# Performance work log

Hardware: AMD Instinct MI355X
Metric: run time of the kernel (lower is better)

## Reference

```python
import jax, jax.numpy as jnp
import numpy as np

B, L, H = 256, 2048, 64

def _min_gru(x, Wz, bz, Wh, bh):
    # x: [B, L, Din] -> h: [B, L, H] via parallel scan of h_t = (1-z_t)*h_{t-1} + z_t*h~_t, h_0 = 0
    z = jax.nn.sigmoid(jnp.einsum('bli,ih->blh', x, Wz) + bz)
    h_tilde = jnp.einsum('bli,ih->blh', x, Wh) + bh
    a = 1.0 - z
    b = z * h_tilde
    def combine(c1, c2):
        a1, b1 = c1
        a2, b2 = c2
        return a1 * a2, b1 * a2 + b2
    _, h = jax.lax.associative_scan(combine, (a, b), axis=1)
    return h

def _stacked(x, Wz0, bz0, Wh0, bh0, Wz1, bz1, Wh1, bh1, Wo, bo):
    h = _min_gru(x, Wz0, bz0, Wh0, bh0)
    h = _min_gru(h, Wz1, bz1, Wh1, bh1)
    return jnp.einsum('blh,ho->blo', h, Wo) + bo  # [B, L, 1]

def setup_inputs():
    key = jax.random.key(0)
    ks = jax.random.split(key, 32)
    inputs = jax.random.bernoulli(ks[0], 0.5, (B, L)).astype(jnp.float32)
    p_array = jax.random.permutation(ks[1], L).astype(jnp.int32)
    def lin(k, fin, fout):
        return (jax.random.normal(k, (fin, fout), jnp.float32) / np.float32(np.sqrt(fin)))
    d = {'inputs': inputs, 'p_array': p_array}
    i = 2
    for r in (1, 2):
        for nm, fin, fout in (('z0', 1, H), ('h0', 1, H), ('z1', H, H), ('h1', H, H), ('o', H, 1)):
            d['w%d%s' % (r, nm)] = lin(ks[i], fin, fout); i += 1
            d['b%d%s' % (r, nm)] = jnp.zeros((fout,), jnp.float32)
    return d

def reference(inputs, p_array, w1z0, b1z0, w1h0, b1h0, w1z1, b1z1, w1h1, b1h1, w1o, b1o,
              w2z0, b2z0, w2h0, b2h0, w2z1, b2z1, w2h1, b2h1, w2o, b2o):
    x = inputs[..., None]                      # [B, L, 1]
    x_sys = _stacked(x, w1z0, b1z0, w1h0, b1h0, w1z1, b1z1, w1h1, b1h1, w1o, b1o)
    x_int = x[:, p_array, :]                   # interleave along sequence dim
    x_p1 = _stacked(x_int, w2z0, b2z0, w2h0, b2h0, w2z1, b2z1, w2h1, b2h1, w2o, b2o)
    x_tx = jnp.concatenate([x_sys, x_p1], axis=2)  # [B, L, 2]
    mean = jnp.mean(x_tx)
    std = jnp.std(x_tx, ddof=1)                # torch.std is unbiased by default
    return (x_tx - mean) / std                 # squeeze(dim=2) is a no-op on size-2 dim
```

## Files before the change

kernel.cpp:

```cpp
#include <hip/hip_runtime.h>

#define BB 256
#define LL 2048
#define HH 64
#define TT 64
#define SS 68
#define NCH (LL / TT)
#define NTOT (BB * LL * 2)

typedef __attribute__((ext_vector_type(8))) short bf16x8;
typedef __attribute__((ext_vector_type(4))) float f32x4;

__device__ __forceinline__ float rcp_(float x) { return __builtin_amdgcn_rcpf(x); }

__device__ __forceinline__ short f2bf_rne(float f) {
    union { float f; unsigned u; } v; v.f = f;
    unsigned r = v.u + 0x7fff + ((v.u >> 16) & 1);
    return (short)(r >> 16);
}

__device__ __forceinline__ unsigned perm_hi16(float f_hi, float f_lo) {
    union { float f; unsigned u; } a, b;
    a.f = f_hi; b.f = f_lo;
    return __builtin_amdgcn_perm(a.u, b.u, 0x07060302u);
}

template<int D>
__device__ __forceinline__ float rshr(float x) {
    union { float f; int i; } u, r;
    u.f = x;
    r.i = __builtin_amdgcn_update_dpp(0, u.i, 0x110 | D, 0xF, 0xF, true);
    return r.f;
}

__device__ __forceinline__ void p1_scan(const unsigned* __restrict__ bw, int c,
                                        float a0v, float b0v, float a1v, float b1v,
                                        int seg, int col0, int lane7,
                                        float& carry, float* sh)
{
    const unsigned bits = (bw[c * 2 + (seg >> 2)] >> ((seg & 3) << 3)) & 0xffu;
    float A = 1.0f, Bv = 0.0f;
    #pragma unroll
    for (int i = 0; i < 8; ++i) {
        const bool on = (bits >> i) & 1u;
        const float a = on ? a1v : a0v;
        const float b = on ? b1v : b0v;
        A  = A * a;
        Bv = fmaf(Bv, a, b);
    }
    {
        const float Au = rshr<1>(A), Bu = rshr<1>(Bv);
        if (seg >= 1) { const float Ac = A; A = Au * Ac; Bv = fmaf(Bu, Ac, Bv); }
    }
    {
        const float Au = rshr<2>(A), Bu = rshr<2>(Bv);
        if (seg >= 2) { const float Ac = A; A = Au * Ac; Bv = fmaf(Bu, Ac, Bv); }
    }
    {
        const float Au = rshr<4>(A), Bu = rshr<4>(Bv);
        if (seg >= 4) { const float Ac = A; A = Au * Ac; Bv = fmaf(Bu, Ac, Bv); }
    }
    float Ae = rshr<1>(A), Be = rshr<1>(Bv);
    if (seg == 0) { Ae = 1.0f; Be = 0.0f; }
    float cc = fmaf(Ae, carry, Be);
    #pragma unroll
    for (int i = 0; i < 8; ++i) {
        const bool on = (bits >> i) & 1u;
        const float a = on ? a1v : a0v;
        const float b = on ? b1v : b0v;
        cc = fmaf(a, cc, b);
        sh[(seg * 8 + i) * SS + col0] = cc;
    }
    carry = __shfl(cc, lane7);
}

__global__ void __launch_bounds__(512)
__attribute__((amdgpu_waves_per_eu(4, 4)))
gru_fused(const float* __restrict__ x, const int* __restrict__ p,
               const float* __restrict__ w1z0, const float* __restrict__ b1z0,
               const float* __restrict__ w1h0, const float* __restrict__ b1h0,
               const float* __restrict__ w1z1, const float* __restrict__ b1z1,
               const float* __restrict__ w1h1, const float* __restrict__ b1h1,
               const float* __restrict__ w1o,  const float* __restrict__ b1o,
               const float* __restrict__ w2z0, const float* __restrict__ b2z0,
               const float* __restrict__ w2h0, const float* __restrict__ b2h0,
               const float* __restrict__ w2z1, const float* __restrict__ b2z1,
               const float* __restrict__ w2h1, const float* __restrict__ b2h1,
               const float* __restrict__ w2o,  const float* __restrict__ b2o,
               float* __restrict__ out, float* __restrict__ ws)
{
    const int  b  = blockIdx.x;
    const bool pm = (blockIdx.y != 0);

    const float* wz0 = pm ? w2z0 : w1z0;
    const float* bz0 = pm ? b2z0 : b1z0;
    const float* wh0 = pm ? w2h0 : w1h0;
    const float* bh0 = pm ? b2h0 : b1h0;
    const float* wz1 = pm ? w2z1 : w1z1;
    const float* bz1 = pm ? b2z1 : b1z1;
    const float* wh1 = pm ? w2h1 : w1h1;
    const float* bh1 = pm ? b2h1 : b1h1;
    const float* wo  = pm ? w2o  : w1o;
    const float* bov = pm ? b2o  : b1o;

    const int tid   = threadIdx.x;
    const int lane  = tid & 63;
    const int tg    = tid >> 6;
    const int tw    = tg & 3;
    const int hw    = tg >> 2;
    const int q     = lane >> 4;
    const int n     = lane & 15;
    const int seg   = lane & 7;
    const int hidx  = (tg << 3) | (lane >> 3);
    const int lane7 = lane | 7;

    __shared__ __align__(16) float s_h[2 * TT * SS];
    __shared__ unsigned long long s_xb[LL / 64];
    __shared__ float2 s_w[2][2][4][32];
    __shared__ float s_o[2][4][16];
    __shared__ float s_red[16];

    const float* xrow = x + (size_t)b * LL;

    #pragma unroll
    for (int g = 0; g < 4; ++g) {
        const int idx = g * 512 + tid;
        const int src = pm ? p[idx] : idx;
        const unsigned long long m = __ballot(xrow[src] != 0.0f);
        if (lane == 0) s_xb[g * 8 + tg] = m;
    }
    const unsigned* bw = (const unsigned*)s_xb;

    const float z0v = rcp_(1.0f + __expf(-bz0[hidx]));
    const float z1v = rcp_(1.0f + __expf(-(wz0[hidx] + bz0[hidx])));
    const float a0v = 1.0f - z0v, b0v = z0v * bh0[hidx];
    const float a1v = 1.0f - z1v, b1v = z1v * (wh0[hidx] + bh0[hidx]);

    float rbz1[2], rbh1[2], rwo4[2];
    #pragma unroll
    for (int ht = 0; ht < 2; ++ht) {
        const int h = hw * 32 + ht * 16 + n;
        rbz1[ht] = bz1[h];
        rbh1[ht] = bh1[h];
        rwo4[ht] = wo[h];
    }
    const float bo = bov[0];

    bf16x8 wfz[2][2], wfh[2][2];
    for (int ks = 0; ks < 2; ++ks) {
        for (int ht = 0; ht < 2; ++ht) {
            #pragma unroll
            for (int j = 0; j < 8; ++j) {
                const int kk = ks * 32 + q * 8 + j;
                const int h  = hw * 32 + ht * 16 + n;
                wfz[ks][ht][j] = f2bf_rne(wz1[kk * HH + h]);
                wfh[ks][ht][j] = f2bf_rne(wh1[kk * HH + h]);
            }
        }
    }

    float carry0 = 0.0f;
    float carry1[2] = {0.0f, 0.0f};
    f32x4 ga[2], gb[2];
    float Aqe[2], Bqe[2];
    float pvo[4] = {0, 0, 0, 0};
    float lsum = 0.0f, lsum2 = 0.0f;
    float* outp = out + (pm ? 1 : 0);
    const int t0 = tw * 16;
    const int col0 = hidx ^ (seg << 2);
    const int sswz = (tw * 2 + (n >> 3)) << 2;

    auto g2_step = [&](int cm) {
        if (cm > 0 && hw == 0 && n == 15) {
            #pragma unroll
            for (int r = 0; r < 4; ++r) {
                const float v = pvo[r] + s_o[(cm - 1) & 1][tw][q * 4 + r] + bo;
                outp[((size_t)b * LL + (cm - 1) * TT + t0 + q * 4 + r) * 2] = v;
                lsum += v;
                lsum2 = fmaf(v, v, lsum2);
            }
        }
        const int buf = cm & 1;
        float Acm[2] = {1, 1}, Bcm[2] = {0, 0};
        float Ap[2], Bp[2];
        #pragma unroll
        for (int w = 0; w < 4; ++w) {
            #pragma unroll
            for (int ht = 0; ht < 2; ++ht) {
                if (w == tw) { Ap[ht] = Acm[ht]; Bp[ht] = Bcm[ht]; }
                const float2 ab = s_w[buf][hw][w][ht * 16 + n];
                Bcm[ht] = fmaf(ab.x, Bcm[ht], ab.y);
                Acm[ht] *= ab.x;
            }
        }
        float vo[4] = {0, 0, 0, 0};
        #pragma unroll
        for (int ht = 0; ht < 2; ++ht) {
            float cc = fmaf(Aqe[ht], fmaf(Ap[ht], carry1[ht], Bp[ht]), Bqe[ht]);
            #pragma unroll
            for (int r = 0; r < 4; ++r) {
                cc = fmaf(ga[ht][r], cc, gb[ht][r]);
                vo[r] = fmaf(cc, rwo4[ht], vo[r]);
            }
            carry1[ht] = fmaf(Acm[ht], carry1[ht], Bcm[ht]);
        }
        #pragma unroll
        for (int r = 0; r < 4; ++r) {
            vo[r] += rshr<1>(vo[r]);
            vo[r] += rshr<2>(vo[r]);
            vo[r] += rshr<4>(vo[r]);
            vo[r] += rshr<8>(vo[r]);
        }
        if (n == 15) {
            if (hw) {
                #pragma unroll
                for (int r = 0; r < 4; ++r) s_o[buf][tw][q * 4 + r] = vo[r];
            } else {
                #pragma unroll
                for (int r = 0; r < 4; ++r) pvo[r] = vo[r];
            }
        }
    };

    __syncthreads();

    p1_scan(bw, 0, a0v, b0v, a1v, b1v, seg, col0, lane7, carry0, s_h);
    __syncthreads();

    for (int c = 0; c < NCH; ++c) {
        const int cp1 = c + 1;

        if (c > 0) g2_step(c - 1);

        {
            #pragma unroll
            for (int ht = 0; ht < 2; ++ht) {
                ga[ht] = (f32x4){rbz1[ht], rbz1[ht], rbz1[ht], rbz1[ht]};
                gb[ht] = (f32x4){rbh1[ht], rbh1[ht], rbh1[ht], rbh1[ht]};
            }
            const float* shR = s_h + (c & 1) * (TT * SS);
            #pragma unroll
            for (int ks = 0; ks < 2; ++ks) {
                const int base = ks * 32 + q * 8;
                const float* rowp = &shR[(t0 + n) * SS];
                const float4 av0 = *(const float4*)(rowp + (base ^ sswz));
                const float4 av1 = *(const float4*)(rowp + ((base + 4) ^ sswz));
                float af[8] = {av0.x, av0.y, av0.z, av0.w, av1.x, av1.y, av1.z, av1.w};
                union { bf16x8 v; unsigned d[4]; } ahi, alo;
                float rem[8];
                #pragma unroll
                for (int j = 0; j < 8; ++j) {
                    union { float f; unsigned u; } uf; uf.f = af[j];
                    union { unsigned u; float f; } hf; hf.u = uf.u & 0xffff0000u;
                    rem[j] = af[j] - hf.f;
                }
                #pragma unroll
                for (int k = 0; k < 4; ++k) {
                    ahi.d[k] = perm_hi16(af[2 * k + 1], af[2 * k]);
                    alo.d[k] = perm_hi16(rem[2 * k + 1], rem[2 * k]);
                }
                #pragma unroll
                for (int ht = 0; ht < 2; ++ht) {
                    ga[ht] = __builtin_amdgcn_mfma_f32_16x16x32_bf16(ahi.v, wfz[ks][ht], ga[ht], 0, 0, 0);
                    ga[ht] = __builtin_amdgcn_mfma_f32_16x16x32_bf16(alo.v, wfz[ks][ht], ga[ht], 0, 0, 0);
                    gb[ht] = __builtin_amdgcn_mfma_f32_16x16x32_bf16(ahi.v, wfh[ks][ht], gb[ht], 0, 0, 0);
                    gb[ht] = __builtin_amdgcn_mfma_f32_16x16x32_bf16(alo.v, wfh[ks][ht], gb[ht], 0, 0, 0);
                }
            }
            #pragma unroll
            for (int ht = 0; ht < 2; ++ht) {
                #pragma unroll
                for (int r = 0; r < 4; ++r) {
                    const float v   = ga[ht][r];
                    const float a   = rcp_(1.0f + __expf(v));
                    const float htl = gb[ht][r];
                    ga[ht][r] = a;
                    gb[ht][r] = fmaf(-a, htl, htl);
                }
            }
            float Aq[2], Bq[2];
            #pragma unroll
            for (int ht = 0; ht < 2; ++ht) {
                float A = 1.0f, B = 0.0f;
                #pragma unroll
                for (int r = 0; r < 4; ++r) {
                    B = fmaf(ga[ht][r], B, gb[ht][r]);
                    A = A * ga[ht][r];
                }
                Aq[ht] = A; Bq[ht] = B;
            }
            #pragma unroll
            for (int ht = 0; ht < 2; ++ht) {
                const float Au = __shfl_up(Aq[ht], 16), Bu = __shfl_up(Bq[ht], 16);
                if (q >= 1) { const float Ac = Aq[ht]; Aq[ht] = Ac * Au; Bq[ht] = fmaf(Ac, Bu, Bq[ht]); }
            }
            #pragma unroll
            for (int ht = 0; ht < 2; ++ht) {
                const float Au = __shfl_up(Aq[ht], 32), Bu = __shfl_up(Bq[ht], 32);
                if (q >= 2) { const float Ac = Aq[ht]; Aq[ht] = Ac * Au; Bq[ht] = fmaf(Ac, Bu, Bq[ht]); }
            }
            #pragma unroll
            for (int ht = 0; ht < 2; ++ht) {
                const float Ae = __shfl_up(Aq[ht], 16), Be = __shfl_up(Bq[ht], 16);
                Aqe[ht] = (q == 0) ? 1.0f : Ae;
                Bqe[ht] = (q == 0) ? 0.0f : Be;
            }
            if (q == 3) {
                #pragma unroll
                for (int ht = 0; ht < 2; ++ht)
                    s_w[c & 1][hw][tw][ht * 16 + n] = make_float2(Aq[ht], Bq[ht]);
            }
        }

        if (cp1 < NCH)
            p1_scan(bw, cp1, a0v, b0v, a1v, b1v, seg, col0, lane7, carry0,
                    s_h + (cp1 & 1) * (TT * SS));

        __syncthreads();
    }

    g2_step(NCH - 1);
    __syncthreads();
    if (hw == 0 && n == 15) {
        #pragma unroll
        for (int r = 0; r < 4; ++r) {
            const float v = pvo[r] + s_o[(NCH - 1) & 1][tw][q * 4 + r] + bo;
            outp[((size_t)b * LL + (NCH - 1) * TT + t0 + q * 4 + r) * 2] = v;
            lsum += v;
            lsum2 = fmaf(v, v, lsum2);
        }
    }

    #pragma unroll
    for (int o = 32; o; o >>= 1) {
        lsum  += __shfl_down(lsum, o);
        lsum2 += __shfl_down(lsum2, o);
    }
    if (lane == 0) { s_red[tg] = lsum; s_red[8 + tg] = lsum2; }
    __syncthreads();
    if (tid == 0) {
        float s = 0.0f, s2 = 0.0f;
        #pragma unroll
        for (int i = 0; i < 8; ++i) { s += s_red[i]; s2 += s_red[8 + i]; }
        const int gb2 = b * 2 + (pm ? 1 : 0);
        ws[2 * gb2]     = s;
        ws[2 * gb2 + 1] = s2;
    }
}

__global__ void normalize_k(float* __restrict__ out, const float* __restrict__ ws)
{
    __shared__ float s_red[8];
    float s = 0.0f, s2 = 0.0f;
    for (int i = threadIdx.x; i < 2 * BB; i += 256) {
        s  += ws[2 * i];
        s2 += ws[2 * i + 1];
    }
    #pragma unroll
    for (int o = 32; o; o >>= 1) {
        s  += __shfl_down(s, o);
        s2 += __shfl_down(s2, o);
    }
    const int wid = threadIdx.x >> 6;
    if ((threadIdx.x & 63) == 0) { s_red[wid] = s; s_red[4 + wid] = s2; }
    __syncthreads();
    const float tot  = s_red[0] + s_red[1] + s_red[2] + s_red[3];
    const float tot2 = s_red[4] + s_red[5] + s_red[6] + s_red[7];
    const float N    = (float)NTOT;
    const float mean = tot / N;
    const float var  = (tot2 - N * mean * mean) / (N - 1.0f);
    const float inv  = rsqrtf(var);

    const int i = blockIdx.x * blockDim.x + threadIdx.x;
    float4* o4 = (float4*)out;
    float4 v = o4[i];
    v.x = (v.x - mean) * inv;
    v.y = (v.y - mean) * inv;
    v.z = (v.z - mean) * inv;
    v.w = (v.w - mean) * inv;
    o4[i] = v;
}

extern "C" void kernel_launch(void* const* d_in, const int* in_sizes, int n_in,
                              void* d_out, int out_size, void* d_ws, size_t ws_size,
                              hipStream_t stream)
{
    (void)in_sizes; (void)n_in; (void)out_size; (void)ws_size;
    const float* x = (const float*)d_in[0];
    const int*   p = (const int*)d_in[1];
    float* out = (float*)d_out;
    float* ws  = (float*)d_ws;

    dim3 grid(BB, 2);
    gru_fused<<<grid, 512, 0, stream>>>(
        x, p,
        (const float*)d_in[2],  (const float*)d_in[3],
        (const float*)d_in[4],  (const float*)d_in[5],
        (const float*)d_in[6],  (const float*)d_in[7],
        (const float*)d_in[8],  (const float*)d_in[9],
        (const float*)d_in[10], (const float*)d_in[11],
        (const float*)d_in[12], (const float*)d_in[13],
        (const float*)d_in[14], (const float*)d_in[15],
        (const float*)d_in[16], (const float*)d_in[17],
        (const float*)d_in[18], (const float*)d_in[19],
        (const float*)d_in[20], (const float*)d_in[21],
        out, ws);

    normalize_k<<<NTOT / 4 / 256, 256, 0, stream>>>(out, ws);
}
```

Before: 184.8 us.

## Reorder chunk loop to overlap next-chunk scan with MFMA, scalarize wave ids

The shared-memory operands for the current chunk are now loaded up front, and the first-layer scan of the next chunk is moved ahead of the second-layer step and MFMA work, so its latency can overlap with them. The per-step select of a/b is cached in registers for reuse in the second pass. The cross-segment carry broadcast uses ds_swizzle instead of a generic shuffle. Wave indices go through readfirstlane so that branches and addressing on them become scalar. The reordering raises register pressure because the loaded tiles and cached coefficients stay live across the scan.

```diff
diff --git a/kernel.cpp b/kernel.cpp
--- a/kernel.cpp
+++ b/kernel.cpp
@@ -11,7 +11,7 @@
 typedef __attribute__((ext_vector_type(8))) short bf16x8;
 typedef __attribute__((ext_vector_type(4))) float f32x4;
 
-__device__ __forceinline__ float rcp_(float x) { return __builtin_amdgcn_rcpf(x); }
+__device__ __forceinline__ float rcp_(float x)  { return __builtin_amdgcn_rcpf(x); }
 
 __device__ __forceinline__ short f2bf_rne(float f) {
     union { float f; unsigned u; } v; v.f = f;
@@ -33,20 +33,28 @@
     return r.f;
 }
 
+__device__ __forceinline__ float bcast7(float x) {
+    union { float f; int i; } u, r;
+    u.f = x;
+    r.i = __builtin_amdgcn_ds_swizzle(u.i, 0x00F8);
+    return r.f;
+}
+
 __device__ __forceinline__ void p1_scan(const unsigned* __restrict__ bw, int c,
                                         float a0v, float b0v, float a1v, float b1v,
-                                        int seg, int col0, int lane7,
+                                        int seg, int col0,
                                         float& carry, float* sh)
 {
     const unsigned bits = (bw[c * 2 + (seg >> 2)] >> ((seg & 3) << 3)) & 0xffu;
+    float ai[8], bi[8];
     float A = 1.0f, Bv = 0.0f;
     #pragma unroll
     for (int i = 0; i < 8; ++i) {
         const bool on = (bits >> i) & 1u;
-        const float a = on ? a1v : a0v;
-        const float b = on ? b1v : b0v;
-        A  = A * a;
-        Bv = fmaf(Bv, a, b);
+        ai[i] = on ? a1v : a0v;
+        bi[i] = on ? b1v : b0v;
+        A  = A * ai[i];
+        Bv = fmaf(Bv, ai[i], bi[i]);
     }
     {
         const float Au = rshr<1>(A), Bu = rshr<1>(Bv);
@@ -65,13 +73,10 @@
     float cc = fmaf(Ae, carry, Be);
     #pragma unroll
     for (int i = 0; i < 8; ++i) {
-        const bool on = (bits >> i) & 1u;
-        const float a = on ? a1v : a0v;
-        const float b = on ? b1v : b0v;
-        cc = fmaf(a, cc, b);
+        cc = fmaf(ai[i], cc, bi[i]);
         sh[(seg * 8 + i) * SS + col0] = cc;
     }
-    carry = __shfl(cc, lane7);
+    carry = bcast7(cc);
 }
 
 __global__ void __launch_bounds__(512)
@@ -106,13 +111,13 @@
     const int tid   = threadIdx.x;
     const int lane  = tid & 63;
     const int tg    = tid >> 6;
-    const int tw    = tg & 3;
-    const int hw    = tg >> 2;
+    const int tgu   = __builtin_amdgcn_readfirstlane(tg);
+    const int twu   = tgu & 3;
+    const int hwu   = tgu >> 2;
     const int q     = lane >> 4;
     const int n     = lane & 15;
     const int seg   = lane & 7;
-    const int hidx  = (tg << 3) | (lane >> 3);
-    const int lane7 = lane | 7;
+    const int hidx  = (tgu << 3) | (lane >> 3);
 
     __shared__ __align__(16) float s_h[2 * TT * SS];
     __shared__ unsigned long long s_xb[LL / 64];
@@ -127,7 +132,7 @@
         const int idx = g * 512 + tid;
         const int src = pm ? p[idx] : idx;
         const unsigned long long m = __ballot(xrow[src] != 0.0f);
-        if (lane == 0) s_xb[g * 8 + tg] = m;
+        if (lane == 0) s_xb[g * 8 + tgu] = m;
     }
     const unsigned* bw = (const unsigned*)s_xb;
 
@@ -139,7 +144,7 @@
     float rbz1[2], rbh1[2], rwo4[2];
     #pragma unroll
     for (int ht = 0; ht < 2; ++ht) {
-        const int h = hw * 32 + ht * 16 + n;
+        const int h = hwu * 32 + ht * 16 + n;
         rbz1[ht] = bz1[h];
         rbh1[ht] = bh1[h];
         rwo4[ht] = wo[h];
@@ -152,7 +157,7 @@
             #pragma unroll
             for (int j = 0; j < 8; ++j) {
                 const int kk = ks * 32 + q * 8 + j;
-                const int h  = hw * 32 + ht * 16 + n;
+                const int h  = hwu * 32 + ht * 16 + n;
                 wfz[ks][ht][j] = f2bf_rne(wz1[kk * HH + h]);
                 wfh[ks][ht][j] = f2bf_rne(wh1[kk * HH + h]);
             }
@@ -166,15 +171,15 @@
     float pvo[4] = {0, 0, 0, 0};
     float lsum = 0.0f, lsum2 = 0.0f;
     float* outp = out + (pm ? 1 : 0);
-    const int t0 = tw * 16;
+    const int t0 = twu * 16;
     const int col0 = hidx ^ (seg << 2);
-    const int sswz = (tw * 2 + (n >> 3)) << 2;
+    const int sswz = (twu * 2 + (n >> 3)) << 2;
 
     auto g2_step = [&](int cm) {
-        if (cm > 0 && hw == 0 && n == 15) {
+        if (cm > 0 && hwu == 0 && n == 15) {
             #pragma unroll
             for (int r = 0; r < 4; ++r) {
-                const float v = pvo[r] + s_o[(cm - 1) & 1][tw][q * 4 + r] + bo;
+                const float v = pvo[r] + s_o[(cm - 1) & 1][twu][q * 4 + r] + bo;
                 outp[((size_t)b * LL + (cm - 1) * TT + t0 + q * 4 + r) * 2] = v;
                 lsum += v;
                 lsum2 = fmaf(v, v, lsum2);
@@ -187,8 +192,8 @@
         for (int w = 0; w < 4; ++w) {
             #pragma unroll
             for (int ht = 0; ht < 2; ++ht) {
-                if (w == tw) { Ap[ht] = Acm[ht]; Bp[ht] = Bcm[ht]; }
-                const float2 ab = s_w[buf][hw][w][ht * 16 + n];
+                if (w == twu) { Ap[ht] = Acm[ht]; Bp[ht] = Bcm[ht]; }
+                const float2 ab = s_w[buf][hwu][w][ht * 16 + n];
                 Bcm[ht] = fmaf(ab.x, Bcm[ht], ab.y);
                 Acm[ht] *= ab.x;
             }
@@ -212,9 +217,9 @@
             vo[r] += rshr<8>(vo[r]);
         }
         if (n == 15) {
-            if (hw) {
-                #pragma unroll
-                for (int r = 0; r < 4; ++r) s_o[buf][tw][q * 4 + r] = vo[r];
+            if (hwu) {
+                #pragma unroll
+                for (int r = 0; r < 4; ++r) s_o[buf][twu][q * 4 + r] = vo[r];
             } else {
                 #pragma unroll
                 for (int r = 0; r < 4; ++r) pvo[r] = vo[r];
@@ -224,12 +229,26 @@
 
     __syncthreads();
 
-    p1_scan(bw, 0, a0v, b0v, a1v, b1v, seg, col0, lane7, carry0, s_h);
+    p1_scan(bw, 0, a0v, b0v, a1v, b1v, seg, col0, carry0, s_h);
     __syncthreads();
 
     for (int c = 0; c < NCH; ++c) {
         const int cp1 = c + 1;
 
+        const float* shR = s_h + (c & 1) * (TT * SS);
+        const float* rowp = &shR[(t0 + n) * SS];
+        float4 L[4];
+        #pragma unroll
+        for (int ks = 0; ks < 2; ++ks) {
+            const int base = ks * 32 + q * 8;
+            L[2 * ks + 0] = *(const float4*)(rowp + (base ^ sswz));
+            L[2 * ks + 1] = *(const float4*)(rowp + ((base + 4) ^ sswz));
+        }
+
+        if (cp1 < NCH)
+            p1_scan(bw, cp1, a0v, b0v, a1v, b1v, seg, col0, carry0,
+                    s_h + (cp1 & 1) * (TT * SS));
+
         if (c > 0) g2_step(c - 1);
 
         {
@@ -238,13 +257,10 @@
                 ga[ht] = (f32x4){rbz1[ht], rbz1[ht], rbz1[ht], rbz1[ht]};
                 gb[ht] = (f32x4){rbh1[ht], rbh1[ht], rbh1[ht], rbh1[ht]};
             }
-            const float* shR = s_h + (c & 1) * (TT * SS);
             #pragma unroll
             for (int ks = 0; ks < 2; ++ks) {
-                const int base = ks * 32 + q * 8;
-                const float* rowp = &shR[(t0 + n) * SS];
-                const float4 av0 = *(const float4*)(rowp + (base ^ sswz));
-                const float4 av1 = *(const float4*)(rowp + ((base + 4) ^ sswz));
+                const float4 av0 = L[2 * ks + 0];
+                const float4 av1 = L[2 * ks + 1];
                 float af[8] = {av0.x, av0.y, av0.z, av0.w, av1.x, av1.y, av1.z, av1.w};
                 union { bf16x8 v; unsigned d[4]; } ahi, alo;
                 float rem[8];
@@ -308,23 +324,19 @@
             if (q == 3) {
                 #pragma unroll
                 for (int ht = 0; ht < 2; ++ht)
-                    s_w[c & 1][hw][tw][ht * 16 + n] = make_float2(Aq[ht], Bq[ht]);
-            }
-        }
-
-        if (cp1 < NCH)
-            p1_scan(bw, cp1, a0v, b0v, a1v, b1v, seg, col0, lane7, carry0,
-                    s_h + (cp1 & 1) * (TT * SS));
+                    s_w[c & 1][hwu][twu][ht * 16 + n] = make_float2(Aq[ht], Bq[ht]);
+            }
+        }
 
         __syncthreads();
     }
 
     g2_step(NCH - 1);
     __syncthreads();
-    if (hw == 0 && n == 15) {
+    if (hwu == 0 && n == 15) {
         #pragma unroll
         for (int r = 0; r < 4; ++r) {
-            const float v = pvo[r] + s_o[(NCH - 1) & 1][tw][q * 4 + r] + bo;
+            const float v = pvo[r] + s_o[(NCH - 1) & 1][twu][q * 4 + r] + bo;
             outp[((size_t)b * LL + (NCH - 1) * TT + t0 + q * 4 + r) * 2] = v;
             lsum += v;
             lsum2 = fmaf(v, v, lsum2);
@@ -336,7 +348,7 @@
         lsum  += __shfl_down(lsum, o);
         lsum2 += __shfl_down(lsum2, o);
     }
-    if (lane == 0) { s_red[tg] = lsum; s_red[8 + tg] = lsum2; }
+    if (lane == 0) { s_red[tgu] = lsum; s_red[8 + tgu] = lsum2; }
     __syncthreads();
     if (tid == 0) {
         float s = 0.0f, s2 = 0.0f;
```

Result: slower. 193.2 us (+4.6%).
